# Kernel optimization log

Measured on AMD Instinct MI355X. Metric: run time of the kernel, lower is better.

The kernel has to match this reference:

```python
import jax, jax.numpy as jnp
import numpy as np

B, L, H, C = 2, 128, 768, 6


def setup_inputs() -> dict:
    key = jax.random.key(0)
    k1, k2, k3 = jax.random.split(key, 3)
    hidden = jax.random.normal(k1, (B, L, H), dtype=jnp.float32)
    attention_mask = jnp.ones((B, L), dtype=jnp.float32)
    cls_w = jax.random.normal(k2, (2 * H, C), dtype=jnp.float32) * 0.02
    cls_b = jnp.zeros((C,), dtype=jnp.float32)
    feat_w = jax.random.normal(k3, (2 * H + 3 * C, 2 * H), dtype=jnp.float32) * 0.02
    feat_b = jnp.zeros((2 * H,), dtype=jnp.float32)
    return {"hidden": hidden, "attention_mask": attention_mask,
            "cls_w": cls_w, "cls_b": cls_b,
            "feat_w": feat_w, "feat_b": feat_b, "nhops": 2}


def reference(hidden, attention_mask, cls_w, cls_b, feat_w, feat_b, nhops):
    b, l, h = hidden.shape
    # grid features: [B, L, L, 2H] = cat(expand, expand.T)
    fa = jnp.broadcast_to(hidden[:, :, None, :], (b, l, l, h))
    features = jnp.concatenate([fa, fa.transpose(0, 2, 1, 3)], axis=3)
    # triu pair mask [B, L, L, 1]
    m = attention_mask[:, :l]
    mask = jnp.triu(m[:, None, :] * m[:, :, None])[..., None]
    logits = features @ cls_w + cls_b  # [B, L, L, C]
    for _ in range(nhops):
        probs = logits
        lm = probs * mask
        # max over rows / cols, then elementwise max (== cat + max over dim3)
        pooled = jnp.maximum(lm.max(axis=1), lm.max(axis=2))  # [B, L, C]
        lg = jnp.broadcast_to(pooled[:, :, None, :], (b, l, l, pooled.shape[-1]))
        new_features = jnp.concatenate(
            [features, lg, lg.transpose(0, 2, 1, 3), probs], axis=3)
        features = new_features @ feat_w + feat_b
        logits = features @ cls_w + cls_b
    return logits
```

## Files before the change

kernel.cpp:

```cpp
#include <hip/hip_runtime.h>
#include <math.h>

#define BB 2
#define LL 128
#define HH 768
#define H2 1536
#define CC 6
#define NTOK (BB * LL)
#define TOKSZ (NTOK * CC)

#define WFC_OFF   0
#define WFWFC_OFF 9216
#define SM_OFF    18432
#define TOK_OFF   18672

__global__ __launch_bounds__(256) void k1_wfc_dots(const float* __restrict__ feat_w,
                                                   const float* __restrict__ cls_w,
                                                   const float* __restrict__ cls_b,
                                                   const float* __restrict__ feat_b,
                                                   float* __restrict__ ws) {
    int blk = blockIdx.x, tid = threadIdx.x;
    int wave = tid >> 6, lane = tid & 63;
    if (blk < H2) {
        float acc[CC] = {};
        const float* arow = feat_w + (size_t)blk * H2;
        for (int r = tid; r < H2; r += 256) {
            float w = arow[r];
            const float* brow = cls_w + r * CC;
#pragma unroll
            for (int c = 0; c < CC; ++c) acc[c] += w * brow[c];
        }
#pragma unroll
        for (int c = 0; c < CC; ++c)
#pragma unroll
            for (int off = 32; off > 0; off >>= 1) acc[c] += __shfl_down(acc[c], off, 64);
        __shared__ float sred[4][CC];
        if (lane == 0)
#pragma unroll
            for (int c = 0; c < CC; ++c) sred[wave][c] = acc[c];
        __syncthreads();
        if (tid < CC)
            ws[WFC_OFF + blk * CC + tid] = sred[0][tid] + sred[1][tid] + sred[2][tid] + sred[3][tid];
    } else {
        int task = blk - H2;
        const float* va;
        int c, outIdx;
        bool add_clsb = false;
        if (task < 108) {
            int m = task / 36, e = task % 36, cp = e / CC;
            c = e % CC;
            int row = (m == 0) ? (H2 + 2 * CC) : ((m == 1) ? H2 : (H2 + CC));
            va = feat_w + (size_t)(row + cp) * H2;
            outIdx = m * 36 + e;
        } else {
            c = task - 108;
            va = feat_b;
            outIdx = 216 + c;
            add_clsb = true;
        }
        float acc = 0.f;
        for (int r = tid; r < H2; r += 256) acc += va[r] * cls_w[r * CC + c];
#pragma unroll
        for (int off = 32; off > 0; off >>= 1) acc += __shfl_down(acc, off, 64);
        __shared__ float sred1[4];
        if (lane == 0) sred1[wave] = acc;
        __syncthreads();
        if (tid == 0) {
            float v = sred1[0] + sred1[1] + sred1[2] + sred1[3];
            if (add_clsb) v += cls_b[c];
            ws[SM_OFF + outIdx] = v;
        }
    }
}

__global__ __launch_bounds__(256) void k2_wfwfc_dots_tok(const float* __restrict__ feat_w,
                                                         const float* __restrict__ cls_w,
                                                         const float* __restrict__ feat_b,
                                                         const float* __restrict__ hidden,
                                                         float* __restrict__ ws) {
    const float* Wfc = ws + WFC_OFF;
    int blk = blockIdx.x, tid = threadIdx.x;
    int wave = tid >> 6, lane = tid & 63;
    if (blk < H2) {
        float acc[CC] = {};
        const float* arow = feat_w + (size_t)blk * H2;
        for (int r = tid; r < H2; r += 256) {
            float w = arow[r];
            const float* brow = Wfc + r * CC;
#pragma unroll
            for (int c = 0; c < CC; ++c) acc[c] += w * brow[c];
        }
#pragma unroll
        for (int c = 0; c < CC; ++c)
#pragma unroll
            for (int off = 32; off > 0; off >>= 1) acc[c] += __shfl_down(acc[c], off, 64);
        __shared__ float sred[4][CC];
        if (lane == 0)
#pragma unroll
            for (int c = 0; c < CC; ++c) sred[wave][c] = acc[c];
        __syncthreads();
        if (tid < CC)
            ws[WFWFC_OFF + blk * CC + tid] = sred[0][tid] + sred[1][tid] + sred[2][tid] + sred[3][tid];
    } else if (blk < H2 + 114) {
        int task = blk - H2;
        const float* va;
        int c, outIdx;
        if (task < 108) {
            int m = task / 36, e = task % 36, cp = e / CC;
            c = e % CC;
            int row = (m == 0) ? (H2 + 2 * CC) : ((m == 1) ? H2 : (H2 + CC));
            va = feat_w + (size_t)(row + cp) * H2;
            outIdx = (m + 3) * 36 + e;
        } else {
            c = task - 108;
            va = feat_b;
            outIdx = 222 + c;
        }
        float acc = 0.f;
        for (int r = tid; r < H2; r += 256) acc += va[r] * Wfc[r * CC + c];
#pragma unroll
        for (int off = 32; off > 0; off >>= 1) acc += __shfl_down(acc, off, 64);
        __shared__ float sred1[4];
        if (lane == 0) sred1[wave] = acc;
        __syncthreads();
        if (tid == 0) ws[SM_OFF + outIdx] = sred1[0] + sred1[1] + sred1[2] + sred1[3];
    } else {
        int tok = blk - (H2 + 114);
        float acc[4][CC] = {};
        const float* hrow = hidden + (size_t)tok * HH;
        for (int k = tid; k < HH; k += 256) {
            float hk = hrow[k];
            const float* c0 = cls_w + k * CC;
            const float* c1 = cls_w + (HH + k) * CC;
            const float* w0 = Wfc + k * CC;
            const float* w1 = Wfc + (HH + k) * CC;
#pragma unroll
            for (int c = 0; c < CC; ++c) {
                acc[0][c] += hk * c0[c];
                acc[1][c] += hk * c1[c];
                acc[2][c] += hk * w0[c];
                acc[3][c] += hk * w1[c];
            }
        }
#pragma unroll
        for (int g = 0; g < 4; ++g)
#pragma unroll
            for (int c = 0; c < CC; ++c)
#pragma unroll
                for (int off = 32; off > 0; off >>= 1) acc[g][c] += __shfl_down(acc[g][c], off, 64);
        __shared__ float sred2[4][4][CC];
        if (lane == 0)
#pragma unroll
            for (int g = 0; g < 4; ++g)
#pragma unroll
                for (int c = 0; c < CC; ++c) sred2[wave][g][c] = acc[g][c];
        __syncthreads();
        if (tid < 24) {
            int g = tid / CC, c = tid % CC;
            ws[TOK_OFF + g * TOKSZ + tok * CC + c] =
                sred2[0][g][c] + sred2[1][g][c] + sred2[2][g][c] + sred2[3][g][c];
        }
    }
}

__global__ __launch_bounds__(512) void k3_plane_out(const float* __restrict__ hidden,
                                                    const float* __restrict__ mask_in,
                                                    const float* __restrict__ cls_b_g,
                                                    const float* __restrict__ ws,
                                                    float* __restrict__ out) {
    const int blk = blockIdx.x;
    const int b = blk >> 7, i = blk & 127;
    const int tid = threadIdx.x;
    const int wave = tid >> 6, lane = tid & 63;

    __shared__ float sm_sh[240];
    __shared__ float cb_sh[CC];
    __shared__ float s2q[4][LL][CC];
    __shared__ float s1red[8][CC];
    __shared__ float s1sh[CC];
    __shared__ float Bfsh[LL][CC];
    __shared__ float Afsh[CC];
    __shared__ float cfsh[CC];
    __shared__ float xw[2][CC + 1];

    if (tid < 240) sm_sh[tid] = ws[SM_OFF + tid];
    if (tid < CC) cb_sh[tid] = cls_b_g[tid];

    {
        const float* Wf2b = ws + WFWFC_OFF + HH * CC;
        int j = tid & 127, quarter = tid >> 7;
        const float* hrow = hidden + ((size_t)(b * LL + j)) * HH + quarter * 192;
        const float* wbase = Wf2b + quarter * 192 * CC;
        float acc[CC] = {};
        for (int k = 0; k < 192; k += 4) {
            float4 hv = *(const float4*)(hrow + k);
            const float* w0 = wbase + k * CC;
#pragma unroll
            for (int c = 0; c < CC; ++c) {
                acc[c] += hv.x * w0[c] + hv.y * w0[CC + c] + hv.z * w0[2 * CC + c] + hv.w * w0[3 * CC + c];
            }
        }
#pragma unroll
        for (int c = 0; c < CC; ++c) s2q[quarter][j][c] = acc[c];
    }
    {
        const float* Wf2t = ws + WFWFC_OFF;
        const float* hrow = hidden + ((size_t)(b * LL + i)) * HH;
        float acc[CC] = {};
        {
            float hk = hrow[tid];
            const float* w = Wf2t + tid * CC;
#pragma unroll
            for (int c = 0; c < CC; ++c) acc[c] += hk * w[c];
        }
        if (tid < 256) {
            float hk = hrow[512 + tid];
            const float* w = Wf2t + (512 + tid) * CC;
#pragma unroll
            for (int c = 0; c < CC; ++c) acc[c] += hk * w[c];
        }
#pragma unroll
        for (int c = 0; c < CC; ++c)
#pragma unroll
            for (int off = 32; off > 0; off >>= 1) acc[c] += __shfl_down(acc[c], off, 64);
        if (lane == 0)
#pragma unroll
            for (int c = 0; c < CC; ++c) s1red[wave][c] = acc[c];
    }
    __syncthreads();
    if (tid < CC) {
        float s = 0.f;
#pragma unroll
        for (int w = 0; w < 8; ++w) s += s1red[w][tid];
        s1sh[tid] = s;
    }
    __syncthreads();

    const int t = tid;
    float p[CC], q[CC], al[CC], be[CC], pool0v[CC], pool1v[CC], gam[CC];
    float prefV[CC], sufV[CC], prefm = 1.f, sufm = 1.f, m_t = 0.f;
    bool mt = false;

    if (tid < LL) {
        m_t = mask_in[b * LL + t];
        mt = (m_t != 0.f);
#pragma unroll
        for (int c = 0; c < CC; ++c) {
            p[c] = ws[TOK_OFF + 0 * TOKSZ + (b * LL + t) * CC + c];
            q[c] = ws[TOK_OFF + 1 * TOKSZ + (b * LL + t) * CC + c];
        }
#pragma unroll
        for (int c = 0; c < CC; ++c) {
            float g = sm_sh[216 + c];
            for (int cp = 0; cp < CC; ++cp) g += cb_sh[cp] * sm_sh[cp * CC + c];
            gam[c] = g;
        }
#pragma unroll
        for (int c = 0; c < CC; ++c) {
            prefV[c] = mt ? p[c] : -INFINITY;
            sufV[c] = mt ? q[c] : -INFINITY;
        }
        prefm = m_t;
        sufm = m_t;
#pragma unroll
        for (int off = 1; off < 64; off <<= 1) {
#pragma unroll
            for (int c = 0; c < CC; ++c) {
                float v = __shfl_up(prefV[c], off, 64);
                if (lane >= off) prefV[c] = fmaxf(prefV[c], v);
                float u = __shfl_down(sufV[c], off, 64);
                if (lane < 64 - off) sufV[c] = fmaxf(sufV[c], u);
            }
            float vm = __shfl_up(prefm, off, 64);
            if (lane >= off) prefm = fminf(prefm, vm);
            float um = __shfl_down(sufm, off, 64);
            if (lane < 64 - off) sufm = fminf(sufm, um);
        }
        if (lane == 63 && wave == 0) {
#pragma unroll
            for (int c = 0; c < CC; ++c) xw[0][c] = prefV[c];
            xw[0][CC] = prefm;
        }
        if (lane == 0 && wave == 1) {
#pragma unroll
            for (int c = 0; c < CC; ++c) xw[1][c] = sufV[c];
            xw[1][CC] = sufm;
        }
    }
    __syncthreads();
    if (tid < LL) {
        if (wave == 1) {
#pragma unroll
            for (int c = 0; c < CC; ++c) prefV[c] = fmaxf(prefV[c], xw[0][c]);
            prefm = fminf(prefm, xw[0][CC]);
        } else {
#pragma unroll
            for (int c = 0; c < CC; ++c) sufV[c] = fmaxf(sufV[c], xw[1][c]);
            sufm = fminf(sufm, xw[1][CC]);
        }
        bool colz = (t < LL - 1) || (prefm == 0.f);
        bool rowz = (t > 0) || (sufm == 0.f);
#pragma unroll
        for (int c = 0; c < CC; ++c) {
            float cm = 0.f, rm = 0.f;
            if (mt) {
                cm = prefV[c] + q[c] + cb_sh[c];
                if (colz) cm = fmaxf(cm, 0.f);
                rm = p[c] + sufV[c] + cb_sh[c];
                if (rowz) rm = fmaxf(rm, 0.f);
            }
            pool0v[c] = fmaxf(cm, rm);
        }
#pragma unroll
        for (int c = 0; c < CC; ++c) {
            al[c] = ws[TOK_OFF + 2 * TOKSZ + (b * LL + t) * CC + c];
            be[c] = ws[TOK_OFF + 3 * TOKSZ + (b * LL + t) * CC + c];
        }
#pragma unroll
        for (int c = 0; c < CC; ++c)
            for (int cp = 0; cp < CC; ++cp) {
                al[c] += pool0v[cp] * sm_sh[36 + cp * CC + c] + p[cp] * sm_sh[cp * CC + c];
                be[c] += pool0v[cp] * sm_sh[72 + cp * CC + c] + q[cp] * sm_sh[cp * CC + c];
            }
#pragma unroll
        for (int c = 0; c < CC; ++c) {
            prefV[c] = mt ? al[c] : -INFINITY;
            sufV[c] = mt ? be[c] : -INFINITY;
        }
#pragma unroll
        for (int off = 1; off < 64; off <<= 1) {
#pragma unroll
            for (int c = 0; c < CC; ++c) {
                float v = __shfl_up(prefV[c], off, 64);
                if (lane >= off) prefV[c] = fmaxf(prefV[c], v);
                float u = __shfl_down(sufV[c], off, 64);
                if (lane < 64 - off) sufV[c] = fmaxf(sufV[c], u);
            }
        }
    }
    __syncthreads();
    if (tid < LL) {
        if (lane == 63 && wave == 0)
#pragma unroll
            for (int c = 0; c < CC; ++c) xw[0][c] = prefV[c];
        if (lane == 0 && wave == 1)
#pragma unroll
            for (int c = 0; c < CC; ++c) xw[1][c] = sufV[c];
    }
    __syncthreads();
    if (tid < LL) {
        if (wave == 1)
#pragma unroll
            for (int c = 0; c < CC; ++c) prefV[c] = fmaxf(prefV[c], xw[0][c]);
        else
#pragma unroll
            for (int c = 0; c < CC; ++c) sufV[c] = fmaxf(sufV[c], xw[1][c]);
        bool colz = (t < LL - 1) || (prefm == 0.f);
        bool rowz = (t > 0) || (sufm == 0.f);
#pragma unroll
        for (int c = 0; c < CC; ++c) {
            float cm = 0.f, rm = 0.f;
            if (mt) {
                cm = prefV[c] + be[c] + gam[c];
                if (colz) cm = fmaxf(cm, 0.f);
                rm = al[c] + sufV[c] + gam[c];
                if (rowz) rm = fmaxf(rm, 0.f);
            }
            pool1v[c] = fmaxf(cm, rm);
        }
#pragma unroll
        for (int c = 0; c < CC; ++c) {
            float Bv = s2q[0][t][c] + s2q[1][t][c] + s2q[2][t][c] + s2q[3][t][c];
            for (int cp = 0; cp < CC; ++cp) {
                Bv += pool0v[cp] * sm_sh[180 + cp * CC + c] + pool1v[cp] * sm_sh[72 + cp * CC + c]
                    + q[cp] * sm_sh[108 + cp * CC + c] + be[cp] * sm_sh[cp * CC + c];
            }
            Bfsh[t][c] = Bv;
        }
        if (t == i) {
#pragma unroll
            for (int c = 0; c < CC; ++c) {
                float A = s1sh[c];
                for (int cp = 0; cp < CC; ++cp) {
                    A += pool0v[cp] * sm_sh[144 + cp * CC + c] + pool1v[cp] * sm_sh[36 + cp * CC + c]
                       + p[cp] * sm_sh[108 + cp * CC + c] + al[cp] * sm_sh[cp * CC + c];
                }
                Afsh[c] = A;
            }
        }
        if (tid == 0) {
#pragma unroll
            for (int c = 0; c < CC; ++c) {
                float f = sm_sh[222 + c] + sm_sh[216 + c];
                for (int cp = 0; cp < CC; ++cp)
                    f += cb_sh[cp] * sm_sh[108 + cp * CC + c] + gam[cp] * sm_sh[cp * CC + c];
                cfsh[c] = f;
            }
        }
    }
    __syncthreads();
    if (tid < (LL * CC) / 4) {
        int r = tid * 4;
        float4 o;
        float* op = &o.x;
#pragma unroll
        for (int k = 0; k < 4; ++k) {
            int idx = r + k;
            int c = idx % CC, j = idx / CC;
            op[k] = Afsh[c] + Bfsh[j][c] + cfsh[c];
        }
        *(float4*)(out + ((size_t)(b * LL + i)) * (LL * CC) + r) = o;
    }
}

extern "C" void kernel_launch(void* const* d_in, const int* in_sizes, int n_in,
                              void* d_out, int out_size, void* d_ws, size_t ws_size,
                              hipStream_t stream) {
    const float* hidden = (const float*)d_in[0];
    const float* attention_mask = (const float*)d_in[1];
    const float* cls_w = (const float*)d_in[2];
    const float* cls_b = (const float*)d_in[3];
    const float* feat_w = (const float*)d_in[4];
    const float* feat_b = (const float*)d_in[5];
    float* out = (float*)d_out;
    float* ws = (float*)d_ws;

    k1_wfc_dots<<<H2 + 114, 256, 0, stream>>>(feat_w, cls_w, cls_b, feat_b, ws);
    k2_wfwfc_dots_tok<<<H2 + 114 + NTOK, 256, 0, stream>>>(feat_w, cls_w, feat_b, hidden, ws);
    k3_plane_out<<<NTOK, 512, 0, stream>>>(hidden, attention_mask, cls_b, ws, out);
}
```

Baseline: 123.3 us.

## Hoist per-token hidden·W projections into separate kernel instead of per-block recompute

Previously every (b,i) block of the plane kernel recomputed the projection of all 128 tokens of its batch onto the fused weight (the s2q term), plus its own row projection. That is a 128-fold redundant GEMV over hidden per batch. A new k3_tok_s kernel computes both projections once per token and stores them in the workspace. The plane kernel now reads those results and drops to 256 threads. This adds an extra kernel launch and a global round-trip in exchange for removing the redundant compute and hidden traffic.

```diff
diff --git a/kernel.cpp b/kernel.cpp
--- a/kernel.cpp
+++ b/kernel.cpp
@@ -163,8 +163,44 @@
     }
 }
 
-__global__ __launch_bounds__(512) void k3_plane_out(const float* __restrict__ hidden,
-                                                    const float* __restrict__ mask_in,
+__global__ __launch_bounds__(256) void k3_tok_s(const float* __restrict__ hidden,
+                                                float* __restrict__ ws) {
+    const float* Wf2 = ws + WFWFC_OFF;
+    int tok = blockIdx.x, tid = threadIdx.x;
+    int wave = tid >> 6, lane = tid & 63;
+    float acc[2][CC] = {};
+    const float* hrow = hidden + (size_t)tok * HH;
+    for (int k = tid; k < HH; k += 256) {
+        float hk = hrow[k];
+        const float* v0 = Wf2 + k * CC;
+        const float* v1 = Wf2 + (HH + k) * CC;
+#pragma unroll
+        for (int c = 0; c < CC; ++c) {
+            acc[0][c] += hk * v0[c];
+            acc[1][c] += hk * v1[c];
+        }
+    }
+#pragma unroll
+    for (int g = 0; g < 2; ++g)
+#pragma unroll
+        for (int c = 0; c < CC; ++c)
+#pragma unroll
+            for (int off = 32; off > 0; off >>= 1) acc[g][c] += __shfl_down(acc[g][c], off, 64);
+    __shared__ float sred[4][2][CC];
+    if (lane == 0)
+#pragma unroll
+        for (int g = 0; g < 2; ++g)
+#pragma unroll
+            for (int c = 0; c < CC; ++c) sred[wave][g][c] = acc[g][c];
+    __syncthreads();
+    if (tid < 12) {
+        int g = tid / CC, c = tid % CC;
+        ws[TOK_OFF + (4 + g) * TOKSZ + tok * CC + c] =
+            sred[0][g][c] + sred[1][g][c] + sred[2][g][c] + sred[3][g][c];
+    }
+}
+
+__global__ __launch_bounds__(256) void k4_plane_out(const float* __restrict__ mask_in,
                                                     const float* __restrict__ cls_b_g,
                                                     const float* __restrict__ ws,
                                                     float* __restrict__ out) {
@@ -175,9 +211,6 @@
 
     __shared__ float sm_sh[240];
     __shared__ float cb_sh[CC];
-    __shared__ float s2q[4][LL][CC];
-    __shared__ float s1red[8][CC];
-    __shared__ float s1sh[CC];
     __shared__ float Bfsh[LL][CC];
     __shared__ float Afsh[CC];
     __shared__ float cfsh[CC];
@@ -185,55 +218,6 @@
 
     if (tid < 240) sm_sh[tid] = ws[SM_OFF + tid];
     if (tid < CC) cb_sh[tid] = cls_b_g[tid];
-
-    {
-        const float* Wf2b = ws + WFWFC_OFF + HH * CC;
-        int j = tid & 127, quarter = tid >> 7;
-        const float* hrow = hidden + ((size_t)(b * LL + j)) * HH + quarter * 192;
-        const float* wbase = Wf2b + quarter * 192 * CC;
-        float acc[CC] = {};
-        for (int k = 0; k < 192; k += 4) {
-            float4 hv = *(const float4*)(hrow + k);
-            const float* w0 = wbase + k * CC;
-#pragma unroll
-            for (int c = 0; c < CC; ++c) {
-                acc[c] += hv.x * w0[c] + hv.y * w0[CC + c] + hv.z * w0[2 * CC + c] + hv.w * w0[3 * CC + c];
-            }
-        }
-#pragma unroll
-        for (int c = 0; c < CC; ++c) s2q[quarter][j][c] = acc[c];
-    }
-    {
-        const float* Wf2t = ws + WFWFC_OFF;
-        const float* hrow = hidden + ((size_t)(b * LL + i)) * HH;
-        float acc[CC] = {};
-        {
-            float hk = hrow[tid];
-            const float* w = Wf2t + tid * CC;
-#pragma unroll
-            for (int c = 0; c < CC; ++c) acc[c] += hk * w[c];
-        }
-        if (tid < 256) {
-            float hk = hrow[512 + tid];
-            const float* w = Wf2t + (512 + tid) * CC;
-#pragma unroll
-            for (int c = 0; c < CC; ++c) acc[c] += hk * w[c];
-        }
-#pragma unroll
-        for (int c = 0; c < CC; ++c)
-#pragma unroll
-            for (int off = 32; off > 0; off >>= 1) acc[c] += __shfl_down(acc[c], off, 64);
-        if (lane == 0)
-#pragma unroll
-            for (int c = 0; c < CC; ++c) s1red[wave][c] = acc[c];
-    }
-    __syncthreads();
-    if (tid < CC) {
-        float s = 0.f;
-#pragma unroll
-        for (int w = 0; w < 8; ++w) s += s1red[w][tid];
-        s1sh[tid] = s;
-    }
     __syncthreads();
 
     const int t = tid;
@@ -370,7 +354,7 @@
         }
 #pragma unroll
         for (int c = 0; c < CC; ++c) {
-            float Bv = s2q[0][t][c] + s2q[1][t][c] + s2q[2][t][c] + s2q[3][t][c];
+            float Bv = ws[TOK_OFF + 5 * TOKSZ + (b * LL + t) * CC + c];
             for (int cp = 0; cp < CC; ++cp) {
                 Bv += pool0v[cp] * sm_sh[180 + cp * CC + c] + pool1v[cp] * sm_sh[72 + cp * CC + c]
                     + q[cp] * sm_sh[108 + cp * CC + c] + be[cp] * sm_sh[cp * CC + c];
@@ -380,7 +364,7 @@
         if (t == i) {
 #pragma unroll
             for (int c = 0; c < CC; ++c) {
-                float A = s1sh[c];
+                float A = ws[TOK_OFF + 4 * TOKSZ + (b * LL + i) * CC + c];
                 for (int cp = 0; cp < CC; ++cp) {
                     A += pool0v[cp] * sm_sh[144 + cp * CC + c] + pool1v[cp] * sm_sh[36 + cp * CC + c]
                        + p[cp] * sm_sh[108 + cp * CC + c] + al[cp] * sm_sh[cp * CC + c];
@@ -427,5 +411,6 @@
 
     k1_wfc_dots<<<H2 + 114, 256, 0, stream>>>(feat_w, cls_w, cls_b, feat_b, ws);
     k2_wfwfc_dots_tok<<<H2 + 114 + NTOK, 256, 0, stream>>>(feat_w, cls_w, feat_b, hidden, ws);
-    k3_plane_out<<<NTOK, 512, 0, stream>>>(hidden, attention_mask, cls_b, ws, out);
+    k3_tok_s<<<NTOK, 256, 0, stream>>>(hidden, ws);
+    k4_plane_out<<<NTOK, 256, 0, stream>>>(attention_mask, cls_b, ws, out);
 }
```

Measured after the change: 99.56 us. 1.24x faster.
